# Kernel tuning notes

Measured on AMD Instinct MI355X. Metric: run time of the kernel, lower is better.

## Reference

```python
import jax, jax.numpy as jnp
import numpy as np
from jax import lax

NPOINT = 1024   # num_points (FPS centroids)
RADIUS = 0.2    # ball-query radius
K = 32          # samples per ball
FILTERS = [64, 64, 128]


def setup_inputs() -> dict:
    key = jax.random.key(0)
    ks = jax.random.split(key, 10)
    B, N, C = 16, 4096, 64
    xyz = jax.random.uniform(ks[0], (B, N, 3), dtype=jnp.float32)   # unit-cube cloud
    points = jax.random.normal(ks[1], (B, N, C), dtype=jnp.float32)
    inp = {"xyz": xyz, "points": points}
    cin = C + 3  # use_xyz=True concatenates relative xyz
    for i, f in enumerate(FILTERS):
        scale = np.sqrt(2.0 / (cin + f)).astype(np.float32)  # glorot_normal
        inp[f"w{i}"] = jax.random.normal(ks[2 + i], (cin, f), dtype=jnp.float32) * scale
        inp[f"b{i}"] = jnp.zeros((f,), dtype=jnp.float32)
        cin = f
    return inp


def farthest_point_sample(xyz, npoint):
    # Serial greedy FPS. xyz: [B,N,3] -> idx [B,npoint] int32
    B, N, _ = xyz.shape

    def body(carry, _):
        dist, far = carry                                   # [B,N], [B]
        centroid = jnp.take_along_axis(xyz, far[:, None, None], axis=1)  # [B,1,3]
        d = jnp.sum((xyz - centroid) ** 2, axis=-1)         # [B,N]
        dist = jnp.minimum(dist, d)
        nxt = jnp.argmax(dist, axis=-1).astype(jnp.int32)
        return (dist, nxt), far

    init = (jnp.full((B, N), 1e10, xyz.dtype), jnp.zeros((B,), jnp.int32))
    _, idxs = lax.scan(body, init, None, length=npoint)
    return idxs.T  # [B,npoint]


def query_ball(radius, nsample, xyz, new_xyz):
    # First-nsample-in-order points within radius; pad with first hit (CUDA semantics).
    B, N, _ = xyz.shape
    d2 = jnp.sum((new_xyz[:, :, None, :] - xyz[:, None, :, :]) ** 2, axis=-1)  # [B,S,N]
    mask = d2 <= radius * radius
    order = jnp.where(mask, jnp.arange(N, dtype=jnp.int32)[None, None, :], N)
    idx_sorted = jnp.sort(order, axis=-1)[..., :nsample]    # first K valid indices
    first = idx_sorted[..., :1]
    first = jnp.where(first < N, first, 0)                  # empty-ball fallback
    return jnp.where(idx_sorted < N, idx_sorted, first)     # [B,S,K]


def reference(xyz, points, w0, b0, w1, b1, w2, b2):
    B, N, _ = xyz.shape
    fps_idx = farthest_point_sample(xyz, NPOINT)                    # [B,S]
    new_xyz = jnp.take_along_axis(xyz, fps_idx[:, :, None], axis=1)  # [B,S,3]
    idx = query_ball(RADIUS, K, xyz, new_xyz)                        # [B,S,K]

    bix = jnp.arange(B)[:, None, None]
    grouped_xyz = xyz[bix, idx] - new_xyz[:, :, None, :]             # [B,S,K,3] recentered
    grouped_pts = points[bix, idx]                                   # [B,S,K,C]
    g = jnp.concatenate([grouped_pts, grouped_xyz], axis=-1)         # [B,S,K,C+3]

    for w, b in ((w0, b0), (w1, b1), (w2, b2)):                      # shared 1x1-conv MLP
        g = jax.nn.relu(jnp.einsum('bskc,cf->bskf', g, w) + b)
    new_points = jnp.max(g, axis=2)                                  # max-pool over ball
    return new_xyz, new_points
```

## Files before the change

### kernel.cpp

```cpp
#include <hip/hip_runtime.h>
#include <stdint.h>

#define BB 16
#define NN 4096
#define CC 64
#define NPOINT 1024
#define KK 32
#define F1 64
#define F2 64
#define F3 128

#define FPS_T 512
#define PPT (NN / FPS_T)

typedef float v2f __attribute__((ext_vector_type(2)));

#if defined(__has_builtin)
#if __has_builtin(__builtin_amdgcn_update_dpp)
#define HAS_DPP 1
#endif
#endif

#ifdef HAS_DPP
template <int CTRL>
__device__ __forceinline__ unsigned long long dpp_move64(unsigned long long k) {
    int lo = __builtin_amdgcn_update_dpp(0, (int)(unsigned)k,         CTRL, 0xF, 0xF, false);
    int hi = __builtin_amdgcn_update_dpp(0, (int)(unsigned)(k >> 32), CTRL, 0xF, 0xF, false);
    return ((unsigned long long)(unsigned)hi << 32) | (unsigned)lo;
}
__device__ __forceinline__ unsigned long long wave_max_key(unsigned long long key) {
    unsigned long long o;
    o = dpp_move64<0x111>(key); if (o > key) key = o;
    o = dpp_move64<0x112>(key); if (o > key) key = o;
    o = dpp_move64<0x114>(key); if (o > key) key = o;
    o = dpp_move64<0x118>(key); if (o > key) key = o;
    o = dpp_move64<0x142>(key); if (o > key) key = o;
    o = dpp_move64<0x143>(key); if (o > key) key = o;
    return key;
}
#else
__device__ __forceinline__ unsigned long long wave_max_key(unsigned long long key) {
#pragma unroll
    for (int off = 32; off > 0; off >>= 1) {
        unsigned long long o = __shfl_xor(key, off, 64);
        if (o > key) key = o;
    }
    return key;
}
#endif

#define SMEM_BYTES 49664

__global__ __launch_bounds__(512)
void fused_kernel(const float* __restrict__ xyz,
                  const float* __restrict__ points,
                  const float* __restrict__ w0, const float* __restrict__ b0,
                  const float* __restrict__ w1, const float* __restrict__ b1,
                  const float* __restrict__ w2, const float* __restrict__ b2,
                  float* __restrict__ out_xyz,
                  float* __restrict__ out_points,
                  int* __restrict__ ctr) {
    __shared__ __align__(16) char smem[SMEM_BYTES];
    const int tid = threadIdx.x;

    if (blockIdx.x < BB) {
        asm volatile("s_setprio 3");
        float* xs = (float*)smem;
        float* ys = xs + NN;
        float* zs = ys + NN;
        unsigned long long (*wred)[FPS_T / 64] =
            (unsigned long long (*)[FPS_T / 64])(smem + 49152);
        float* cbuf = (float*)(smem + 49280);

        const int b = blockIdx.x;
        const int lane = tid & 63, wid = tid >> 6;
        const float* __restrict__ xb = xyz + (size_t)b * (NN * 3);

        v2f px2[4], py2[4], pz2[4], dd[4];
#pragma unroll
        for (int j = 0; j < 4; ++j) {
#pragma unroll
            for (int h = 0; h < 2; ++h) {
                int p = tid + (2 * j + h) * FPS_T;
                float x = xb[p * 3 + 0];
                float y = xb[p * 3 + 1];
                float z = xb[p * 3 + 2];
                px2[j][h] = x; py2[j][h] = y; pz2[j][h] = z;
                xs[p] = x; ys[p] = y; zs[p] = z;
            }
            dd[j] = (v2f){1e10f, 1e10f};
        }
        __syncthreads();

        float cx = xs[0], cy = ys[0], cz = zs[0];
        float* xo = out_xyz + (size_t)b * NPOINT * 3;

        for (int i = 0; i < NPOINT; ++i) {
            if (tid == 0) {
                cbuf[(i & 7) * 3 + 0] = cx;
                cbuf[(i & 7) * 3 + 1] = cy;
                cbuf[(i & 7) * 3 + 2] = cz;
            }
            {
#pragma clang fp contract(off)
                v2f c2x = (v2f){cx, cx}, c2y = (v2f){cy, cy}, c2z = (v2f){cz, cz};
#pragma unroll
                for (int j = 0; j < 4; ++j) {
                    v2f dx = px2[j] - c2x;
                    v2f dy = py2[j] - c2y;
                    v2f dz = pz2[j] - c2z;
                    v2f ss = (dx * dx + dy * dy) + dz * dz;
                    dd[j] = __builtin_elementwise_min(dd[j], ss);
                }
            }
            v2f m01 = __builtin_elementwise_max(dd[0], dd[1]);
            v2f m23 = __builtin_elementwise_max(dd[2], dd[3]);
            v2f mm  = __builtin_elementwise_max(m01, m23);
            float bd = fmaxf(mm.x, mm.y);
            int bp = 0;
#pragma unroll
            for (int j = 3; j >= 0; --j) {
                if (dd[j].y == bd) bp = tid + (2 * j + 1) * FPS_T;
                if (dd[j].x == bd) bp = tid + (2 * j + 0) * FPS_T;
            }
            unsigned long long key = (((unsigned long long)__float_as_uint(bd)) << 32)
                                   | (unsigned int)(NN - 1 - bp);
            key = wave_max_key(key);
            if (lane == 63) wred[i & 1][wid] = key;
            __syncthreads();

            unsigned long long best = wred[i & 1][0];
#pragma unroll
            for (int w = 1; w < FPS_T / 64; ++w) {
                unsigned long long o = wred[i & 1][w];
                if (o > best) best = o;
            }
            int bi = (NN - 1) - (int)(best & 0xffffffffu);

            if (tid == 0 && (i & 7) == 7) {
                const float4* src = (const float4*)cbuf;
                float4* dst = (float4*)(xo + (size_t)(i - 7) * 3);
                dst[0] = src[0]; dst[1] = src[1]; dst[2] = src[2];
                dst[3] = src[3]; dst[4] = src[4]; dst[5] = src[5];
                __hip_atomic_store(&ctr[b * 16], i + 1,
                                   __ATOMIC_RELEASE, __HIP_MEMORY_SCOPE_AGENT);
            }
            cx = xs[bi]; cy = ys[bi]; cz = zs[bi];
        }
    } else {
        float (*gbuf)[68] = (float (*)[68])smem;
        float (*hbuf)[F1] = (float (*)[F1])(smem + 8704);
        float (*pmax)[F3] = (float (*)[F3])(smem + 16896);
        unsigned long long* cmask = (unsigned long long*)(smem + 20992);
        int* nbr = (int*)(smem + 21504);
        float* wbuf = (float*)(smem + 21632);
        float4* wbuf4 = (float4*)wbuf;

        const int gi = blockIdx.x - BB;
        const int s = gi >> 4;
        const int b = gi & 15;
        const int g = b * NPOINT + s;
        const int f = tid & 63;
        const int wid = tid >> 6;

        {
            const float4* src = (const float4*)w0;
#pragma unroll
            for (int i = tid; i < 1072; i += 512) wbuf4[i] = src[i];
        }

        if (tid == 0) {
            while (__hip_atomic_load(&ctr[b * 16], __ATOMIC_RELAXED,
                                     __HIP_MEMORY_SCOPE_AGENT) < s + 1)
                __builtin_amdgcn_s_sleep(2);
            (void)__hip_atomic_load(&ctr[b * 16], __ATOMIC_ACQUIRE,
                                    __HIP_MEMORY_SCOPE_AGENT);
        }
        __syncthreads();

        unsigned int ux = __hip_atomic_load((unsigned int*)&out_xyz[(size_t)g * 3 + 0],
                                            __ATOMIC_RELAXED, __HIP_MEMORY_SCOPE_AGENT);
        unsigned int uy = __hip_atomic_load((unsigned int*)&out_xyz[(size_t)g * 3 + 1],
                                            __ATOMIC_RELAXED, __HIP_MEMORY_SCOPE_AGENT);
        unsigned int uz = __hip_atomic_load((unsigned int*)&out_xyz[(size_t)g * 3 + 2],
                                            __ATOMIC_RELAXED, __HIP_MEMORY_SCOPE_AGENT);
        const float cx = __uint_as_float(ux);
        const float cy = __uint_as_float(uy);
        const float cz = __uint_as_float(uz);

        {
            const float* __restrict__ xb = xyz + (size_t)b * (NN * 3);
#pragma unroll
            for (int j = 0; j < 8; ++j) {
                int chunk = wid * 8 + j;
                int p = chunk * 64 + f;
                float x = xb[p * 3 + 0];
                float y = xb[p * 3 + 1];
                float z = xb[p * 3 + 2];
                float dx = __fsub_rn(cx, x);
                float dy = __fsub_rn(cy, y);
                float dz = __fsub_rn(cz, z);
                float d2 = __fadd_rn(__fadd_rn(__fmul_rn(dx, dx), __fmul_rn(dy, dy)),
                                     __fmul_rn(dz, dz));
                unsigned long long m = __ballot(d2 <= 0.04f);
                if (f == 0) cmask[chunk] = m;
            }
        }
        __syncthreads();

        if (tid < 64) {
            unsigned long long m = cmask[tid];
            int cnt = (int)__popcll(m);
            int v = cnt;
#pragma unroll
            for (int off = 1; off < 64; off <<= 1) {
                int u = __shfl_up(v, off, 64);
                if (tid >= off) v += u;
            }
            int excl = v - cnt;
            int total = __shfl(v, 63, 64);
            unsigned long long mm = m;
            int r = excl;
            while (mm && r < KK) {
                int bpos = __ffsll(mm) - 1;
                mm &= mm - 1;
                nbr[r++] = tid * 64 + bpos;
            }
            if (total < KK) {
                unsigned long long nz = __ballot(cnt > 0);
                int fchunk = __ffsll(nz) - 1;
                unsigned long long fm = cmask[fchunk];
                int first = fchunk * 64 + __ffsll(fm) - 1;
                if (tid >= total && tid < KK) nbr[tid] = first;
            }
        }
        __syncthreads();

        {
            const float* __restrict__ pb = points + (size_t)b * NN * CC;
#pragma unroll
            for (int m = 0; m < 4; ++m) {
                int k = wid + 8 * m;
                int idx = nbr[k] & (NN - 1);
                gbuf[k][f] = pb[(size_t)idx * CC + f];
            }
            if (tid < 96) {
                int k = tid & 31, q = tid >> 5;
                int idx = nbr[k] & (NN - 1);
                float v = xyz[((size_t)b * NN + idx) * 3 + q];
                float cq = (q == 0) ? cx : ((q == 1) ? cy : cz);
                gbuf[k][CC + q] = __fsub_rn(v, cq);
            }
        }
        __syncthreads();

        v2f acc2[4];

#pragma unroll
        for (int m = 0; m < 4; ++m) acc2[m] = (v2f){0.0f, 0.0f};
#pragma unroll 4
        for (int c4 = 0; c4 < 64; c4 += 4) {
            v2f w01 = (v2f){wbuf[(c4 + 0) * F1 + f], wbuf[(c4 + 1) * F1 + f]};
            v2f w23 = (v2f){wbuf[(c4 + 2) * F1 + f], wbuf[(c4 + 3) * F1 + f]};
#pragma unroll
            for (int m = 0; m < 4; ++m) {
                float4 gv = *(const float4*)&gbuf[wid + 8 * m][c4];
                acc2[m] = __builtin_elementwise_fma((v2f){gv.x, gv.y}, w01, acc2[m]);
                acc2[m] = __builtin_elementwise_fma((v2f){gv.z, gv.w}, w23, acc2[m]);
            }
        }
        {
            float wv0 = wbuf[64 * F1 + f];
            float wv1 = wbuf[65 * F1 + f];
            float wv2 = wbuf[66 * F1 + f];
            float bb = b0[f];
#pragma unroll
            for (int m = 0; m < 4; ++m) {
                int k = wid + 8 * m;
                float a = acc2[m].x + acc2[m].y;
                a = fmaf(gbuf[k][64], wv0, a);
                a = fmaf(gbuf[k][65], wv1, a);
                a = fmaf(gbuf[k][66], wv2, a);
                hbuf[k][f] = fmaxf(a + bb, 0.0f);
            }
        }
        __syncthreads();

        {
            const float4* src = (const float4*)w1;
#pragma unroll
            for (int i = tid; i < 1024; i += 512) wbuf4[i] = src[i];
        }
        __syncthreads();

#pragma unroll
        for (int m = 0; m < 4; ++m) acc2[m] = (v2f){0.0f, 0.0f};
#pragma unroll 4
        for (int c4 = 0; c4 < 64; c4 += 4) {
            v2f w01 = (v2f){wbuf[(c4 + 0) * F2 + f], wbuf[(c4 + 1) * F2 + f]};
            v2f w23 = (v2f){wbuf[(c4 + 2) * F2 + f], wbuf[(c4 + 3) * F2 + f]};
#pragma unroll
            for (int m = 0; m < 4; ++m) {
                float4 gv = *(const float4*)&hbuf[wid + 8 * m][c4];
                acc2[m] = __builtin_elementwise_fma((v2f){gv.x, gv.y}, w01, acc2[m]);
                acc2[m] = __builtin_elementwise_fma((v2f){gv.z, gv.w}, w23, acc2[m]);
            }
        }
        {
            float bb = b1[f];
#pragma unroll
            for (int m = 0; m < 4; ++m)
                gbuf[wid + 8 * m][f] = fmaxf(acc2[m].x + acc2[m].y + bb, 0.0f);
        }
        __syncthreads();

#pragma unroll
        for (int h = 0; h < 2; ++h) {
            {
                const float4* src = (const float4*)w2;
#pragma unroll
                for (int i = tid; i < 1024; i += 512) {
                    int c = i >> 4, col4 = i & 15;
                    wbuf4[i] = src[c * 32 + 16 * h + col4];
                }
            }
            __syncthreads();
#pragma unroll
            for (int m = 0; m < 4; ++m) acc2[m] = (v2f){0.0f, 0.0f};
#pragma unroll 4
            for (int c4 = 0; c4 < 64; c4 += 4) {
                v2f w01 = (v2f){wbuf[(c4 + 0) * 64 + f], wbuf[(c4 + 1) * 64 + f]};
                v2f w23 = (v2f){wbuf[(c4 + 2) * 64 + f], wbuf[(c4 + 3) * 64 + f]};
#pragma unroll
                for (int m = 0; m < 4; ++m) {
                    float4 gv = *(const float4*)&gbuf[wid + 8 * m][c4];
                    acc2[m] = __builtin_elementwise_fma((v2f){gv.x, gv.y}, w01, acc2[m]);
                    acc2[m] = __builtin_elementwise_fma((v2f){gv.z, gv.w}, w23, acc2[m]);
                }
            }
            {
                float pm = -1e30f;
#pragma unroll
                for (int m = 0; m < 4; ++m) pm = fmaxf(pm, acc2[m].x + acc2[m].y);
                pmax[wid][f + 64 * h] = pm;
            }
            __syncthreads();
        }

        if (tid < F3) {
            float v = pmax[0][tid];
#pragma unroll
            for (int w = 1; w < 8; ++w) v = fmaxf(v, pmax[w][tid]);
            v = fmaxf(v + b2[tid], 0.0f);
            out_points[(size_t)g * F3 + tid] = v;
        }
    }
}

extern "C" void kernel_launch(void* const* d_in, const int* in_sizes, int n_in,
                              void* d_out, int out_size, void* d_ws, size_t ws_size,
                              hipStream_t stream) {
    const float* xyz    = (const float*)d_in[0];
    const float* points = (const float*)d_in[1];
    const float* w0 = (const float*)d_in[2];
    const float* b0 = (const float*)d_in[3];
    const float* w1 = (const float*)d_in[4];
    const float* b1 = (const float*)d_in[5];
    const float* w2 = (const float*)d_in[6];
    const float* b2 = (const float*)d_in[7];

    float* out_xyz    = (float*)d_out;
    float* out_points = out_xyz + (size_t)BB * NPOINT * 3;
    int*   ctr        = (int*)d_ws;

    fused_kernel<<<BB + BB * NPOINT, 512, 0, stream>>>(
        xyz, points, w0, b0, w1, b1, w2, b2, out_xyz, out_points, ctr);
}
```

Before: 836.8 us.

## Read MLP weights directly from global, batch FPS centroid publishing by 32, adaptive spin

The grouping/MLP blocks no longer stage w0, w1 and w2 into shared memory. They read the weights straight from global memory (cache-resident), which drops several staging loops and __syncthreads barriers, and layer 3 computes both 64-column halves in a single pass. The FPS blocks now publish centroids and bump the progress counter every 32 iterations instead of every 8. Consumers spin with a longer sleep when they are far behind. Together this cuts FPS-side store and atomic traffic and consumer polling, at the cost of coarser-grained wakeups for the MLP blocks and global-cache weight loads inside the inner loops.

```diff
diff --git a/kernel.cpp b/kernel.cpp
--- a/kernel.cpp
+++ b/kernel.cpp
@@ -97,9 +97,9 @@
 
         for (int i = 0; i < NPOINT; ++i) {
             if (tid == 0) {
-                cbuf[(i & 7) * 3 + 0] = cx;
-                cbuf[(i & 7) * 3 + 1] = cy;
-                cbuf[(i & 7) * 3 + 2] = cz;
+                cbuf[(i & 31) * 3 + 0] = cx;
+                cbuf[(i & 31) * 3 + 1] = cy;
+                cbuf[(i & 31) * 3 + 2] = cz;
             }
             {
 #pragma clang fp contract(off)
@@ -137,11 +137,11 @@
             }
             int bi = (NN - 1) - (int)(best & 0xffffffffu);
 
-            if (tid == 0 && (i & 7) == 7) {
+            if (tid == 0 && (i & 31) == 31) {
                 const float4* src = (const float4*)cbuf;
-                float4* dst = (float4*)(xo + (size_t)(i - 7) * 3);
-                dst[0] = src[0]; dst[1] = src[1]; dst[2] = src[2];
-                dst[3] = src[3]; dst[4] = src[4]; dst[5] = src[5];
+                float4* dst = (float4*)(xo + (size_t)(i - 31) * 3);
+#pragma unroll
+                for (int q = 0; q < 24; ++q) dst[q] = src[q];
                 __hip_atomic_store(&ctr[b * 16], i + 1,
                                    __ATOMIC_RELEASE, __HIP_MEMORY_SCOPE_AGENT);
             }
@@ -153,8 +153,6 @@
         float (*pmax)[F3] = (float (*)[F3])(smem + 16896);
         unsigned long long* cmask = (unsigned long long*)(smem + 20992);
         int* nbr = (int*)(smem + 21504);
-        float* wbuf = (float*)(smem + 21632);
-        float4* wbuf4 = (float4*)wbuf;
 
         const int gi = blockIdx.x - BB;
         const int s = gi >> 4;
@@ -163,16 +161,14 @@
         const int f = tid & 63;
         const int wid = tid >> 6;
 
-        {
-            const float4* src = (const float4*)w0;
-#pragma unroll
-            for (int i = tid; i < 1072; i += 512) wbuf4[i] = src[i];
-        }
-
         if (tid == 0) {
-            while (__hip_atomic_load(&ctr[b * 16], __ATOMIC_RELAXED,
-                                     __HIP_MEMORY_SCOPE_AGENT) < s + 1)
-                __builtin_amdgcn_s_sleep(2);
+            const int target = s + 1;
+            int c;
+            while ((c = __hip_atomic_load(&ctr[b * 16], __ATOMIC_RELAXED,
+                                          __HIP_MEMORY_SCOPE_AGENT)) < target) {
+                if (target - c > 64) __builtin_amdgcn_s_sleep(64);
+                else                 __builtin_amdgcn_s_sleep(4);
+            }
             (void)__hip_atomic_load(&ctr[b * 16], __ATOMIC_ACQUIRE,
                                     __HIP_MEMORY_SCOPE_AGENT);
         }
@@ -260,19 +256,19 @@
         for (int m = 0; m < 4; ++m) acc2[m] = (v2f){0.0f, 0.0f};
 #pragma unroll 4
         for (int c4 = 0; c4 < 64; c4 += 4) {
-            v2f w01 = (v2f){wbuf[(c4 + 0) * F1 + f], wbuf[(c4 + 1) * F1 + f]};
-            v2f w23 = (v2f){wbuf[(c4 + 2) * F1 + f], wbuf[(c4 + 3) * F1 + f]};
+            v2f wA = (v2f){w0[(c4 + 0) * F1 + f], w0[(c4 + 1) * F1 + f]};
+            v2f wB = (v2f){w0[(c4 + 2) * F1 + f], w0[(c4 + 3) * F1 + f]};
 #pragma unroll
             for (int m = 0; m < 4; ++m) {
                 float4 gv = *(const float4*)&gbuf[wid + 8 * m][c4];
-                acc2[m] = __builtin_elementwise_fma((v2f){gv.x, gv.y}, w01, acc2[m]);
-                acc2[m] = __builtin_elementwise_fma((v2f){gv.z, gv.w}, w23, acc2[m]);
-            }
-        }
-        {
-            float wv0 = wbuf[64 * F1 + f];
-            float wv1 = wbuf[65 * F1 + f];
-            float wv2 = wbuf[66 * F1 + f];
+                acc2[m] = __builtin_elementwise_fma((v2f){gv.x, gv.y}, wA, acc2[m]);
+                acc2[m] = __builtin_elementwise_fma((v2f){gv.z, gv.w}, wB, acc2[m]);
+            }
+        }
+        {
+            float wv0 = w0[64 * F1 + f];
+            float wv1 = w0[65 * F1 + f];
+            float wv2 = w0[66 * F1 + f];
             float bb = b0[f];
 #pragma unroll
             for (int m = 0; m < 4; ++m) {
@@ -286,24 +282,17 @@
         }
         __syncthreads();
 
-        {
-            const float4* src = (const float4*)w1;
-#pragma unroll
-            for (int i = tid; i < 1024; i += 512) wbuf4[i] = src[i];
-        }
-        __syncthreads();
-
 #pragma unroll
         for (int m = 0; m < 4; ++m) acc2[m] = (v2f){0.0f, 0.0f};
 #pragma unroll 4
         for (int c4 = 0; c4 < 64; c4 += 4) {
-            v2f w01 = (v2f){wbuf[(c4 + 0) * F2 + f], wbuf[(c4 + 1) * F2 + f]};
-            v2f w23 = (v2f){wbuf[(c4 + 2) * F2 + f], wbuf[(c4 + 3) * F2 + f]};
+            v2f wA = (v2f){w1[(c4 + 0) * F2 + f], w1[(c4 + 1) * F2 + f]};
+            v2f wB = (v2f){w1[(c4 + 2) * F2 + f], w1[(c4 + 3) * F2 + f]};
 #pragma unroll
             for (int m = 0; m < 4; ++m) {
                 float4 gv = *(const float4*)&hbuf[wid + 8 * m][c4];
-                acc2[m] = __builtin_elementwise_fma((v2f){gv.x, gv.y}, w01, acc2[m]);
-                acc2[m] = __builtin_elementwise_fma((v2f){gv.z, gv.w}, w23, acc2[m]);
+                acc2[m] = __builtin_elementwise_fma((v2f){gv.x, gv.y}, wA, acc2[m]);
+                acc2[m] = __builtin_elementwise_fma((v2f){gv.z, gv.w}, wB, acc2[m]);
             }
         }
         {
@@ -314,39 +303,35 @@
         }
         __syncthreads();
 
-#pragma unroll
-        for (int h = 0; h < 2; ++h) {
-            {
-                const float4* src = (const float4*)w2;
-#pragma unroll
-                for (int i = tid; i < 1024; i += 512) {
-                    int c = i >> 4, col4 = i & 15;
-                    wbuf4[i] = src[c * 32 + 16 * h + col4];
-                }
-            }
-            __syncthreads();
-#pragma unroll
-            for (int m = 0; m < 4; ++m) acc2[m] = (v2f){0.0f, 0.0f};
-#pragma unroll 4
-            for (int c4 = 0; c4 < 64; c4 += 4) {
-                v2f w01 = (v2f){wbuf[(c4 + 0) * 64 + f], wbuf[(c4 + 1) * 64 + f]};
-                v2f w23 = (v2f){wbuf[(c4 + 2) * 64 + f], wbuf[(c4 + 3) * 64 + f]};
-#pragma unroll
-                for (int m = 0; m < 4; ++m) {
-                    float4 gv = *(const float4*)&gbuf[wid + 8 * m][c4];
-                    acc2[m] = __builtin_elementwise_fma((v2f){gv.x, gv.y}, w01, acc2[m]);
-                    acc2[m] = __builtin_elementwise_fma((v2f){gv.z, gv.w}, w23, acc2[m]);
-                }
-            }
-            {
-                float pm = -1e30f;
-#pragma unroll
-                for (int m = 0; m < 4; ++m) pm = fmaxf(pm, acc2[m].x + acc2[m].y);
-                pmax[wid][f + 64 * h] = pm;
-            }
-            __syncthreads();
-        }
-
+        v2f a0[4], a1[4];
+#pragma unroll
+        for (int m = 0; m < 4; ++m) { a0[m] = (v2f){0.f, 0.f}; a1[m] = (v2f){0.f, 0.f}; }
+#pragma unroll 2
+        for (int c4 = 0; c4 < 64; c4 += 4) {
+            v2f wA0 = (v2f){w2[(c4 + 0) * F3 + f],      w2[(c4 + 1) * F3 + f]};
+            v2f wB0 = (v2f){w2[(c4 + 2) * F3 + f],      w2[(c4 + 3) * F3 + f]};
+            v2f wA1 = (v2f){w2[(c4 + 0) * F3 + f + 64], w2[(c4 + 1) * F3 + f + 64]};
+            v2f wB1 = (v2f){w2[(c4 + 2) * F3 + f + 64], w2[(c4 + 3) * F3 + f + 64]};
+#pragma unroll
+            for (int m = 0; m < 4; ++m) {
+                float4 gv = *(const float4*)&gbuf[wid + 8 * m][c4];
+                a0[m] = __builtin_elementwise_fma((v2f){gv.x, gv.y}, wA0, a0[m]);
+                a0[m] = __builtin_elementwise_fma((v2f){gv.z, gv.w}, wB0, a0[m]);
+                a1[m] = __builtin_elementwise_fma((v2f){gv.x, gv.y}, wA1, a1[m]);
+                a1[m] = __builtin_elementwise_fma((v2f){gv.z, gv.w}, wB1, a1[m]);
+            }
+        }
+        {
+            float pm0 = -1e30f, pm1 = -1e30f;
+#pragma unroll
+            for (int m = 0; m < 4; ++m) {
+                pm0 = fmaxf(pm0, a0[m].x + a0[m].y);
+                pm1 = fmaxf(pm1, a1[m].x + a1[m].y);
+            }
+            pmax[wid][f] = pm0;
+            pmax[wid][f + 64] = pm1;
+        }
+        __syncthreads();
         if (tid < F3) {
             float v = pmax[0][tid];
 #pragma unroll
```

Result: faster. 820.1 us (-2.0%).
